# Optimization experiments

Hardware: AMD Instinct MI355X
Metric: run time of the kernel (lower is better)

The kernel has to match this reference:

```python
import jax, jax.numpy as jnp
import numpy as np

B, L, D = 2, 2048, 1024
H = 16
C = 128            # chunk_size
N = L // C         # num chunks
SCALE = float(np.sqrt(D))  # softmax_scale = sqrt(d_model)


def setup_inputs() -> dict:
    key = jax.random.key(0)
    ks = jax.random.split(key, 5)
    return {
        "x": jax.random.normal(ks[0], (B, L, D), dtype=jnp.float32),
        "w_qkv": jax.random.normal(ks[1], (D, 3 * D), dtype=jnp.float32) * (1.0 / np.sqrt(D)),
        "b_qkv": jax.random.normal(ks[2], (3 * D,), dtype=jnp.float32) * 0.02,
        "w_o": jax.random.normal(ks[3], (D, D), dtype=jnp.float32) * (1.0 / np.sqrt(D)),
        "b_o": jax.random.normal(ks[4], (D,), dtype=jnp.float32) * 0.02,
    }


def reference(x, w_qkv, b_qkv, w_o, b_o):
    b, l, d = x.shape
    hd = d // H
    qkv = x @ w_qkv + b_qkv                         # (B,L,3D)
    q, k, v = jnp.split(qkv, 3, axis=-1)
    q = q.reshape(b, l, H, hd)
    k = k.reshape(b, l, H, hd)
    v = v.reshape(b, l, H, hd)

    q_chunks = q.reshape(b, N, C, H, hd)
    k_chunks = k.reshape(b, N, C, H, hd)
    # mean_pool over the chunk dim
    q_pool = q_chunks.mean(axis=2)                  # (B,N,H,hd)
    k_pool = k_chunks.mean(axis=2)

    token2chunk = jnp.einsum('blhd,bnhd->bhln', q, k_pool)          # (B,H,L,N)
    chunk2token = jnp.einsum('bnhd,bnchd->bhnc', q_pool, k_chunks)  # (B,H,N,C)
    # outer product over (n,c) -> full (B,H,L,L) score matrix
    A = token2chunk[..., :, None] * chunk2token[:, :, None, :, :]   # (B,H,L,N,C)
    A = A.reshape(b, H, l, l)

    # direct intra-chunk attention overwrites the diagonal blocks
    direct = jnp.einsum('bnqhd,bnkhd->bhnqk', q_chunks, k_chunks)   # (B,H,N,C,C)
    A6 = A.reshape(b, H, N, C, N, C)
    eye = jnp.eye(N, dtype=bool)[:, None, :, None]                  # (N,1,N,1)
    A6 = jnp.where(eye, direct[:, :, :, :, None, :], A6)
    A = A6.reshape(b, H, l, l)

    # causal mask applied multiplicatively (masked scores become 0, NOT -inf)
    causal = jnp.tril(jnp.ones((l, l), dtype=bool))
    A = jnp.where(causal, A, 0.0) / SCALE
    A = jax.nn.softmax(A, axis=-1)

    out = jnp.einsum('bhqv,bvhd->bhqd', A, v)       # (B,H,L,hd)
    out = out.transpose(0, 2, 1, 3).reshape(b, l, d)
    return out @ w_o + b_o
```

## Files before the change

kernel.cpp:

```cpp
#include <hip/hip_runtime.h>
#include <math.h>

#define B_   2
#define L_   2048
#define D_   1024
#define H_   16
#define HD_  64
#define C_   128
#define N_   16
#define INV_SCALE 0.03125f
#define SCL2 0.0450842200f

typedef _Float16 h8 __attribute__((ext_vector_type(8)));
typedef _Float16 h4 __attribute__((ext_vector_type(4)));
typedef float    f4 __attribute__((ext_vector_type(4)));

#define MFMA16(a, b, c) __builtin_amdgcn_mfma_f32_16x16x32_f16((a), (b), (c), 0, 0, 0)

#if __has_builtin(__builtin_amdgcn_exp2f)
#define EXP2(x) __builtin_amdgcn_exp2f(x)
#else
#define EXP2(x) exp2f(x)
#endif

__device__ __forceinline__ void gl_lds16(const void* g, void* l) {
  __builtin_amdgcn_global_load_lds(
      (const __attribute__((address_space(1))) void*)g,
      (__attribute__((address_space(3))) void*)l, 16, 0, 0);
}

#define SBAR()  do { __builtin_amdgcn_sched_barrier(0); \
                     __builtin_amdgcn_s_barrier();      \
                     __builtin_amdgcn_sched_barrier(0); } while (0)
#define LGKM0() do { asm volatile("s_waitcnt lgkmcnt(0)" ::: "memory"); \
                     __builtin_amdgcn_sched_barrier(0); } while (0)
#define VMW(n)  do { asm volatile("s_waitcnt vmcnt(" #n ")" ::: "memory"); \
                     __builtin_amdgcn_sched_barrier(0); } while (0)

__global__ __launch_bounds__(256) void prep_kernel(
    const float* __restrict__ X, _Float16* __restrict__ Xh,
    const float* __restrict__ Wq, _Float16* __restrict__ WqT,
    const float* __restrict__ Wo, _Float16* __restrict__ WoT)
{
  __shared__ float ts[32][36];
  const int tid = threadIdx.x;
  const int id = blockIdx.x;
  if (id < 4096) {
    int i = id * 1024 + tid * 4;
    float4 v = *(const float4*)(X + i);
    h4 o = { (_Float16)v.x, (_Float16)v.y, (_Float16)v.z, (_Float16)v.w };
    *(h4*)(Xh + i) = o;
    return;
  }
  const float* W; _Float16* WT; int Nc, bx, by;
  if (id < 7168) {
    int idx = id - 4096;
    W = Wq; WT = WqT; Nc = 3072; bx = idx % 96; by = idx / 96;
  } else {
    int idx = id - 7168;
    W = Wo; WT = WoT; Nc = 1024; bx = idx & 31; by = idx >> 5;
  }
  const int n0 = bx * 32, k0 = by * 32;
  {
    int kr = tid >> 3, nc4 = (tid & 7) * 4;
    float4 v = *(const float4*)&W[(size_t)(k0 + kr) * Nc + n0 + nc4];
    ts[kr][nc4+0] = v.x; ts[kr][nc4+1] = v.y; ts[kr][nc4+2] = v.z; ts[kr][nc4+3] = v.w;
  }
  __syncthreads();
  {
    int nr = tid >> 3, kc4 = (tid & 7) * 4;
    h4 o = { (_Float16)ts[kc4+0][nr], (_Float16)ts[kc4+1][nr],
             (_Float16)ts[kc4+2][nr], (_Float16)ts[kc4+3][nr] };
    *(h4*)&WT[(size_t)(n0 + nr) * 1024 + k0 + kc4] = o;
  }
}

__global__ __launch_bounds__(512, 2) void qkv256_kernel(
    const _Float16* __restrict__ A, const _Float16* __restrict__ Bt,
    const float* __restrict__ bias,
    _Float16* __restrict__ Qh, _Float16* __restrict__ Kh, _Float16* __restrict__ VT,
    float* __restrict__ QP, float* __restrict__ KP, float* __restrict__ VCS)
{
  __shared__ __align__(16) _Float16 As[2][16384];
  __shared__ __align__(16) _Float16 Bs[2][12288];

  const int tid = threadIdx.x;
  const int w = tid >> 6, lane = tid & 63;
  const int q = lane >> 4, r = lane & 15, r7 = r & 7;
  const int wm = w >> 2, wn = w & 3;

  const int id = blockIdx.x, xcd = id & 7, slot = id >> 3;
  const int m0 = ((xcd >> 1) * 4 + (slot & 3)) * 256;
  const int n0 = ((xcd & 1) * 8 + (slot >> 2)) * 192;

  const int srow = tid >> 3;
  const int spart = (tid & 7) ^ (srow & 7);
  const _Float16* Asrc = A  + (size_t)(m0 + srow) * 1024 + spart * 8;
  const _Float16* Bsrc = Bt + (size_t)(n0 + srow) * 1024 + spart * 8;
  const int ldst = w * 512;

  const int aoffb = (wm * 128 + r) * 64;
  const int boffb = (wn * 48 + r) * 64;
  const int k0s = (q ^ r7) << 3;
  const int k1s = ((4 + q) ^ r7) << 3;

  auto stA = [&](int cc, int ko, int qq) {
    gl_lds16(Asrc + (size_t)qq * 65536 + ko, &As[cc][qq * 4096 + ldst]);
  };
  auto stB = [&](int cc, int ko, int qq) {
    gl_lds16(Bsrc + (size_t)qq * 65536 + ko, &Bs[cc][qq * 4096 + ldst]);
  };

  f4 acc[8][3];
  #pragma unroll
  for (int m = 0; m < 8; ++m)
    #pragma unroll
    for (int n = 0; n < 3; ++n) acc[m][n] = (f4){0.f, 0.f, 0.f, 0.f};

  stB(0, 0, 0); stB(0, 0, 1); stB(0, 0, 2);
  stA(0, 0, 0); stA(0, 0, 2); stA(0, 0, 1); stA(0, 0, 3);
  VMW(2);
  SBAR();

  for (int t = 0; t < 16; ++t) {
    const int c = t & 1;
    const _Float16* __restrict__ Ab = As[c];
    const _Float16* __restrict__ Bb = Bs[c];
    const int kt = (t + 1) << 6;
    const bool pf = (t < 15);
    h8 af[4], bf[3];

    #pragma unroll
    for (int m = 0; m < 4; ++m) af[m] = *(const h8*)&Ab[aoffb + m * 1024 + k0s];
    #pragma unroll
    for (int n = 0; n < 3; ++n) bf[n] = *(const h8*)&Bb[boffb + n * 1024 + k0s];
    if (pf) { stB(c ^ 1, kt, 0); stB(c ^ 1, kt, 1); }
    SBAR();
    LGKM0();
    __builtin_amdgcn_s_setprio(1);
    #pragma unroll
    for (int m = 0; m < 4; ++m)
      #pragma unroll
      for (int n = 0; n < 3; ++n) acc[m][n] = MFMA16(af[m], bf[n], acc[m][n]);
    __builtin_amdgcn_s_setprio(0);
    __builtin_amdgcn_sched_barrier(0);
    if (pf) { VMW(2); } else { VMW(0); }
    SBAR();

    #pragma unroll
    for (int m = 0; m < 4; ++m) af[m] = *(const h8*)&Ab[aoffb + (4 + m) * 1024 + k0s];
    if (pf) { stB(c ^ 1, kt, 2); stA(c ^ 1, kt, 0); }
    SBAR();
    LGKM0();
    __builtin_amdgcn_s_setprio(1);
    #pragma unroll
    for (int m = 0; m < 4; ++m)
      #pragma unroll
      for (int n = 0; n < 3; ++n) acc[4 + m][n] = MFMA16(af[m], bf[n], acc[4 + m][n]);
    __builtin_amdgcn_s_setprio(0);
    __builtin_amdgcn_sched_barrier(0);
    SBAR();

    #pragma unroll
    for (int m = 0; m < 4; ++m) af[m] = *(const h8*)&Ab[aoffb + m * 1024 + k1s];
    #pragma unroll
    for (int n = 0; n < 3; ++n) bf[n] = *(const h8*)&Bb[boffb + n * 1024 + k1s];
    if (pf) { stA(c ^ 1, kt, 2); stA(c ^ 1, kt, 1); }
    SBAR();
    LGKM0();
    __builtin_amdgcn_s_setprio(1);
    #pragma unroll
    for (int m = 0; m < 4; ++m)
      #pragma unroll
      for (int n = 0; n < 3; ++n) acc[m][n] = MFMA16(af[m], bf[n], acc[m][n]);
    __builtin_amdgcn_s_setprio(0);
    __builtin_amdgcn_sched_barrier(0);
    SBAR();

    #pragma unroll
    for (int m = 0; m < 4; ++m) af[m] = *(const h8*)&Ab[aoffb + (4 + m) * 1024 + k1s];
    if (pf) {
      stA(c ^ 1, kt, 3);
      VMW(2);
    }
    SBAR();
    LGKM0();
    __builtin_amdgcn_s_setprio(1);
    #pragma unroll
    for (int m = 0; m < 4; ++m)
      #pragma unroll
      for (int n = 0; n < 3; ++n) acc[4 + m][n] = MFMA16(af[m], bf[n], acc[4 + m][n]);
    __builtin_amdgcn_s_setprio(0);
    __builtin_amdgcn_sched_barrier(0);
    SBAR();
  }

  const int rb = m0 + wm * 128;
  const int b2 = rb >> 11;
  const int nch = (rb & 2047) >> 7;
  #pragma unroll
  for (int tc = 0; tc < 3; ++tc) {
    const int gn = n0 + wn * 48 + tc * 16 + r;
    const float bj = bias[gn];
    const int which = gn >> 10, rem = gn & 1023;
    const int h2 = rem >> 6, d2 = rem & 63;
    if (which < 2) {
      _Float16* dst = which == 0 ? Qh : Kh;
      #pragma unroll
      for (int m = 0; m < 8; ++m)
        #pragma unroll
        for (int i = 0; i < 4; ++i) {
          const int gm = rb + m * 16 + q * 4 + i;
          const int l2 = gm & 2047;
          dst[(((size_t)(b2 * H_ + h2)) * L_ + l2) * HD_ + d2] =
              (_Float16)(acc[m][tc][i] + bj);
        }
    } else {
      #pragma unroll
      for (int m = 0; m < 8; ++m) {
        const int gm0 = rb + m * 16 + q * 4;
        const int l2 = gm0 & 2047;
        h4 hv = { (_Float16)(acc[m][tc][0] + bj), (_Float16)(acc[m][tc][1] + bj),
                  (_Float16)(acc[m][tc][2] + bj), (_Float16)(acc[m][tc][3] + bj) };
        *(h4*)&VT[((size_t)(b2 * H_ + h2) * HD_ + d2) * L_ + l2] = hv;
      }
    }
    float s2 = 0.f;
    #pragma unroll
    for (int m = 0; m < 8; ++m)
      #pragma unroll
      for (int i = 0; i < 4; ++i) s2 += acc[m][tc][i];
    s2 += __shfl_xor(s2, 16);
    s2 += __shfl_xor(s2, 32);
    if (q == 0) {
      const size_t o = (((size_t)(b2 * H_ + h2)) * N_ + nch) * HD_ + d2;
      if (which == 0)      QP[o] = s2 * (1.f / 128.f) + bj;
      else if (which == 1) KP[o] = s2 * (1.f / 128.f) + bj;
      else                 VCS[o] = s2 + 128.f * bj;
    }
  }
}

template<int MT>
__global__ __launch_bounds__(256, 4) void gemm16_kernel(
    const _Float16* __restrict__ A, const _Float16* __restrict__ Bt,
    const float* __restrict__ bias,
    _Float16* __restrict__ Qh, _Float16* __restrict__ Kh, _Float16* __restrict__ VT,
    float* __restrict__ out,
    float* __restrict__ QP, float* __restrict__ KP, float* __restrict__ VCS,
    int Kd, int mode)
{
  constexpr int SM = MT / 32;
  __shared__ __align__(16) _Float16 As[2][MT * 32];
  __shared__ __align__(16) _Float16 Bs[2][4096];
  __shared__ float cred[2][128];
  const int tid = threadIdx.x;
  const int lane = tid & 63, w = tid >> 6;
  const int q = lane >> 4, r = lane & 15;
  const int mb = (w >> 1) * (MT / 2);
  const int nb = (w & 1) * 64;

  int m0, n0;
  {
    const int id = blockIdx.x;
    const int xcd = id & 7, slot = id >> 3;
    if constexpr (MT == 128) {
      n0 = (xcd * 3 + (slot % 3)) * 128;
      m0 = (slot / 3) * 128;
    } else {
      m0 = (xcd * 8 + (slot >> 3)) * 64;
      n0 = (slot & 7) * 128;
    }
  }

  const int Rr = tid >> 2;
  const int cd = (tid & 3) ^ ((Rr >> 1) & 3);
  const _Float16* Ag = A + (size_t)(m0 + Rr) * Kd + cd * 8;
  const _Float16* Bg = Bt + (size_t)(n0 + Rr) * Kd + cd * 8;
  const size_t rowStep = (size_t)64 * Kd;

  f4 acc[SM][4];
  #pragma unroll
  for (int s = 0; s < SM; ++s)
    #pragma unroll
    for (int t = 0; t < 4; ++t) acc[s][t] = (f4){0.f, 0.f, 0.f, 0.f};

  const int nIter = Kd >> 5;
  const int koff = (q ^ ((r >> 1) & 3)) << 3;

  auto stage = [&](int bf, int kt) {
    _Float16* Asl = &As[bf][w * 512];
    _Float16* Bsl = &Bs[bf][w * 512];
    gl_lds16(Ag + kt, Asl);
    if constexpr (MT == 128) gl_lds16(Ag + kt + rowStep, Asl + 2048);
    gl_lds16(Bg + kt, Bsl);
    gl_lds16(Bg + kt + rowStep, Bsl + 2048);
  };

  stage(0, 0);

  for (int it = 0; it < nIter; ++it) {
    __syncthreads();
    if (it + 1 < nIter) stage((it + 1) & 1, (it + 1) << 5);
    const _Float16* Ab = As[it & 1];
    const _Float16* Bb = Bs[it & 1];
    h8 af[SM], bf4[4];
    #pragma unroll
    for (int s = 0; s < SM; ++s)
      af[s] = *(const h8*)&Ab[(mb + s * 16 + r) * 32 + koff];
    #pragma unroll
    for (int t = 0; t < 4; ++t)
      bf4[t] = *(const h8*)&Bb[(nb + t * 16 + r) * 32 + koff];
    #pragma unroll
    for (int s = 0; s < SM; ++s)
      #pragma unroll
      for (int t = 0; t < 4; ++t)
        acc[s][t] = MFMA16(af[s], bf4[t], acc[s][t]);
  }

  if (mode == 0) {
    #pragma unroll
    for (int t = 0; t < 4; ++t) {
      int gn = n0 + nb + t * 16 + r;
      float bj = bias[gn];
      int which = gn >> 10, rem = gn & 1023;
      int h2 = rem >> 6, d2 = rem & 63;
      if (which < 2) {
        _Float16* dst = which == 0 ? Qh : Kh;
        #pragma unroll
        for (int s = 0; s < SM; ++s)
          #pragma unroll
          for (int i = 0; i < 4; ++i) {
            int gm = m0 + mb + s * 16 + q * 4 + i;
            int b2 = gm >> 11, l2 = gm & 2047;
            dst[(((size_t)(b2 * H_ + h2)) * L_ + l2) * HD_ + d2] =
                (_Float16)(acc[s][t][i] + bj);
          }
      } else {
        #pragma unroll
        for (int s = 0; s < SM; ++s) {
          int gm0 = m0 + mb + s * 16 + q * 4;
          int b2 = gm0 >> 11, l2 = gm0 & 2047;
          h4 hv = { (_Float16)(acc[s][t][0] + bj), (_Float16)(acc[s][t][1] + bj),
                    (_Float16)(acc[s][t][2] + bj), (_Float16)(acc[s][t][3] + bj) };
          *(h4*)&VT[((size_t)(b2 * H_ + h2) * HD_ + d2) * L_ + l2] = hv;
        }
      }
    }
    float colsum[4];
    #pragma unroll
    for (int t = 0; t < 4; ++t) {
      float s2 = 0.f;
      #pragma unroll
      for (int s = 0; s < SM; ++s)
        #pragma unroll
        for (int i = 0; i < 4; ++i) s2 += acc[s][t][i];
      s2 += __shfl_xor(s2, 16);
      s2 += __shfl_xor(s2, 32);
      colsum[t] = s2;
    }
    if (q == 0) {
      #pragma unroll
      for (int t = 0; t < 4; ++t)
        cred[w >> 1][nb + t * 16 + r] = colsum[t];
    }
    __syncthreads();
    if (tid < 128) {
      int jj = tid;
      float ssum = cred[0][jj] + cred[1][jj];
      int gn = n0 + jj;
      float bj = bias[gn];
      int which = gn >> 10, rem = gn & 1023;
      int h2 = rem >> 6, d2 = rem & 63;
      int b2 = m0 >> 11, nch = (m0 & 2047) >> 7;
      size_t o = (((size_t)(b2 * H_ + h2)) * N_ + nch) * HD_ + d2;
      if (which == 0)      QP[o] = ssum * (1.f / 128.f) + bj;
      else if (which == 1) KP[o] = ssum * (1.f / 128.f) + bj;
      else                 VCS[o] = ssum + 128.f * bj;
    }
  } else {
    #pragma unroll
    for (int t = 0; t < 4; ++t) {
      int gn = n0 + nb + t * 16 + r;
      float bj = bias[gn];
      #pragma unroll
      for (int s = 0; s < SM; ++s)
        #pragma unroll
        for (int i = 0; i < 4; ++i) {
          int gm = m0 + mb + s * 16 + q * 4 + i;
          out[(size_t)gm * 1024 + gn] = acc[s][t][i] + bj;
        }
    }
  }
}

__global__ __launch_bounds__(128) void pool2_kernel(
    const float* __restrict__ QP, const _Float16* __restrict__ Kh,
    const float* __restrict__ VCS,
    float* __restrict__ C2T, float* __restrict__ C2TMX, float* __restrict__ C2TMN,
    float* __restrict__ CSUF)
{
  __shared__ float qp_s[64];
  __shared__ float red[4];
  if (blockIdx.x >= 512) {
    int bh = blockIdx.x - 512, d = threadIdx.x;
    if (d < 64) {
      float run = 0.f;
      for (int n = N_ - 1; n >= 0; --n) {
        size_t o = ((size_t)bh * N_ + n) * HD_ + d;
        CSUF[o] = run;
        run += VCS[o];
      }
    }
    return;
  }
  int bh = blockIdx.x >> 4, n = blockIdx.x & 15, tid = threadIdx.x;
  int w = tid >> 6, lane = tid & 63;
  if (tid < 64) qp_s[tid] = QP[((size_t)bh * N_ + n) * HD_ + tid];
  const _Float16* kr = Kh + (((size_t)bh * L_) + n * C_ + tid) * HD_;
  h8 kv[8];
  #pragma unroll
  for (int c8 = 0; c8 < 8; ++c8) kv[c8] = *(const h8*)(kr + c8 * 8);
  __syncthreads();
  float s = 0.f;
  #pragma unroll
  for (int c8 = 0; c8 < 8; ++c8)
    #pragma unroll
    for (int j = 0; j < 8; ++j)
      s = fmaf((float)kv[c8][j], qp_s[c8 * 8 + j], s);
  C2T[((size_t)bh * N_ + n) * C_ + tid] = s;
  float mx = s, mn = s;
  #pragma unroll
  for (int st = 1; st <= 32; st <<= 1) {
    mx = fmaxf(mx, __shfl_xor(mx, st));
    mn = fminf(mn, __shfl_xor(mn, st));
  }
  if (lane == 0) { red[w * 2] = mx; red[w * 2 + 1] = mn; }
  __syncthreads();
  if (tid == 0) {
    C2TMX[bh * N_ + n] = fmaxf(red[0], red[2]);
    C2TMN[bh * N_ + n] = fminf(red[1], red[3]);
  }
}

__global__ __launch_bounds__(512, 4) void attn4_kernel(
    const _Float16* __restrict__ Qh, const _Float16* __restrict__ Kh,
    const _Float16* __restrict__ VT,
    const float* __restrict__ C2T, const float* __restrict__ C2TMX,
    const float* __restrict__ C2TMN, const float* __restrict__ CSUF,
    const float* __restrict__ KP, _Float16* __restrict__ AOh)
{
  __shared__ __align__(16) _Float16 buf0[8192];
  __shared__ __align__(16) _Float16 buf1[8192];
  __shared__ __align__(16) _Float16 buf2[8192];
  __shared__ __align__(16) _Float16 kp_s[1024];
  __shared__ __align__(16) float c2t_s[2][128];

  const int tid = threadIdx.x;
  const int w = tid >> 6, lane = tid & 63;
  const int q = lane >> 4, r = lane & 15;
  const int r7 = r & 7;
  const int id = blockIdx.x;
  const int bh = ((id & 7) << 2) + ((id >> 3) & 3);
  const int nq = 15 - (id >> 5);
  const int l0 = nq * 128;
  const int rowA = l0 + w * 16 + r;
  const int pcw = w * 16 + r;
  const size_t bhL = (size_t)bh * L_;
  const int b2 = bh >> 4, h2 = bh & 15;

  auto stageV = [&](_Float16* buf, int n) {
    #pragma unroll
    for (int j2 = 0; j2 < 2; ++j2) {
      int f = j2 * 512 + tid;
      int d = f >> 4, p = f & 15;
      int c16 = p ^ (d & 7);
      gl_lds16(VT + ((size_t)bh * HD_ + d) * L_ + n * C_ + c16 * 8,
               buf + (size_t)(j2 * 512 + w * 64) * 8);
    }
  };
  auto stageK = [&](_Float16* buf, int n) {
    #pragma unroll
    for (int j2 = 0; j2 < 2; ++j2) {
      int f = j2 * 512 + tid;
      int c = f >> 3, p = f & 7;
      int ck = p ^ (c & 7);
      gl_lds16(Kh + (bhL + n * C_ + c) * HD_ + ck * 8,
               buf + (size_t)(j2 * 512 + w * 64) * 8);
    }
  };
  auto stageC = [&](int bf, int n) {
    if (tid < 32)
      gl_lds16(C2T + ((size_t)bh * N_ + n) * C_ + tid * 4, &c2t_s[bf][0]);
  };

  if (tid < 256) {
    int n4 = tid >> 4, d4 = (tid & 15) * 4;
    float4 kpv = *(const float4*)&KP[((size_t)bh * N_ + n4) * HD_ + d4];
    int sd = ((((d4 >> 3) ^ (n4 & 7)) << 3) | (d4 & 7));
    h4 hv = { (_Float16)kpv.x, (_Float16)kpv.y, (_Float16)kpv.z, (_Float16)kpv.w };
    *(h4*)&kp_s[n4 * 64 + sd] = hv;
  }
  h8 qa0 = *(const h8*)(Qh + (bhL + rowA) * HD_ + q * 8);
  h8 qa1 = *(const h8*)(Qh + (bhL + rowA) * HD_ + 32 + q * 8);
  float mxL = C2TMX[bh * N_ + r];
  float mnL = C2TMN[bh * N_ + r];
  stageK(buf0, nq);
  stageV(buf2, nq);
  if (nq >= 1) stageC(0, nq - 1);
  __syncthreads();

  f4 tvacc = (f4){0.f, 0.f, 0.f, 0.f};
  {
    h8 kpa0 = *(const h8*)&kp_s[r * 64 + ((q ^ r7) << 3)];
    h8 kpa1 = *(const h8*)&kp_s[r * 64 + (((4 + q) ^ r7) << 3)];
    tvacc = MFMA16(kpa0, qa0, tvacc);
    tvacc = MFMA16(kpa1, qa1, tvacc);
  }
  float tvs[4];
  #pragma unroll
  for (int i = 0; i < 4; ++i) tvs[i] = tvacc[i] * SCL2;

  float pm = -1e30f;
  #pragma unroll
  for (int i = 0; i < 4; ++i) {
    int n = q * 4 + i;
    float mx = __shfl(mxL, n);
    float mn = __shfl(mnL, n);
    float cm = fmaxf(tvs[i] * mx, tvs[i] * mn);
    pm = (n < nq) ? fmaxf(pm, cm) : pm;
  }
  pm = fmaxf(pm, __shfl_xor(pm, 16));
  pm = fmaxf(pm, __shfl_xor(pm, 32));

  f4 sc[8];
  #pragma unroll
  for (int u = 0; u < 8; ++u) sc[u] = (f4){0.f, 0.f, 0.f, 0.f};
  {
    h8 kc0 = *(const h8*)&buf0[r * 64 + ((q ^ r7) << 3)];
    h8 kc1 = *(const h8*)&buf0[r * 64 + (((4 + q) ^ r7) << 3)];
    #pragma unroll
    for (int u = 0; u < 8; ++u) {
      h8 kn0, kn1;
      if (u < 7) {
        kn0 = *(const h8*)&buf0[((u + 1) * 16 + r) * 64 + ((q ^ r7) << 3)];
        kn1 = *(const h8*)&buf0[((u + 1) * 16 + r) * 64 + (((4 + q) ^ r7) << 3)];
      }
      sc[u] = MFMA16(kc0, qa0, sc[u]);
      sc[u] = MFMA16(kc1, qa1, sc[u]);
      kc0 = kn0; kc1 = kn1;
    }
  }

  float rm = -1e30f;
  #pragma unroll
  for (int u = 0; u < 8; ++u)
    #pragma unroll
    for (int i = 0; i < 4; ++i) {
      int lcol = u * 16 + q * 4 + i;
      float v = sc[u][i] * SCL2;
      v = (lcol <= pcw) ? v : -1e30f;
      sc[u][i] = v;
      rm = fmaxf(rm, v);
    }
  rm = fmaxf(rm, __shfl_xor(rm, 16));
  rm = fmaxf(rm, __shfl_xor(rm, 32));

  const float M = fmaxf(fmaxf(pm, rm), 0.f);
  const float e0 = EXP2(-M);

  __syncthreads();

  _Float16* pw = (w < 4) ? (buf0 + w * 2048) : (buf1 + (w - 4) * 2048);
  const int pwbase = r * 128 + ((q & 1) << 2);
  float csl = 0.f;
  #pragma unroll
  for (int u = 0; u < 8; ++u) {
    h4 pv4;
    #pragma unroll
    for (int i = 0; i < 4; ++i) {
      float v = sc[u][i];
      float p = (v > -1e29f) ? EXP2(v - M) : 0.f;
      csl += p;
      pv4[i] = (_Float16)p;
    }
    *(h4*)&pw[pwbase + ((((u << 1) | (q >> 1)) ^ r7) << 3)] = pv4;
  }
  csl += __shfl_xor(csl, 16);
  csl += __shfl_xor(csl, 32);
  float den = csl;

  f4 oacc[4], sacc[4];
  #pragma unroll
  for (int t = 0; t < 4; ++t) {
    oacc[t] = (f4){0.f, 0.f, 0.f, 0.f};
    sacc[t] = (f4){0.f, 0.f, 0.f, 0.f};
  }
  {
    h8 pcur = *(const h8*)&pw[r * 128 + ((q ^ r7) << 3)];
    h8 vcur[4];
    #pragma unroll
    for (int t = 0; t < 4; ++t)
      vcur[t] = *(const h8*)&buf2[(t * 16 + r) * 128 + ((q ^ r7) << 3)];
    #pragma unroll
    for (int s = 0; s < 4; ++s) {
      h8 pnxt; h8 vnxt[4];
      if (s < 3) {
        pnxt = *(const h8*)&pw[r * 128 + ((((s + 1) * 4 + q) ^ r7) << 3)];
        #pragma unroll
        for (int t = 0; t < 4; ++t)
          vnxt[t] = *(const h8*)&buf2[(t * 16 + r) * 128 + ((((s + 1) * 4 + q) ^ r7) << 3)];
      }
      h8 mk;
      #pragma unroll
      for (int j2 = 0; j2 < 8; ++j2)
        mk[j2] = (_Float16)((s * 32 + q * 8 + j2 > pcw) ? 1.f : 0.f);
      #pragma unroll
      for (int t = 0; t < 4; ++t) {
        oacc[t] = MFMA16(pcur, vcur[t], oacc[t]);
        sacc[t] = MFMA16(mk, vcur[t], sacc[t]);
      }
      pcur = pnxt;
      #pragma unroll
      for (int t = 0; t < 4; ++t) vcur[t] = vnxt[t];
    }
  }

  __syncthreads();
  if (nq >= 1) stageV(buf1, nq - 1);

  float dsum = 0.f;
  const float negM = -M;
  for (int n = nq - 1; n >= 0; --n) {
    const int k = nq - 1 - n;
    const _Float16* curb = (k & 1) ? buf2 : buf1;
    __syncthreads();
    if (n >= 1) {
      stageV((k & 1) ? buf1 : buf2, n - 1);
      stageC((k + 1) & 1, n - 1);
    }
    int i0 = n & 3;
    float tvx = i0 == 0 ? tvs[0] : i0 == 1 ? tvs[1] : i0 == 2 ? tvs[2] : tvs[3];
    float tvn = __shfl(tvx, ((n >> 2) << 4) + r);
    const float* c2p = c2t_s[k & 1];

    f4 cca = *(const f4*)&c2p[q * 8];
    f4 ccb = *(const f4*)&c2p[q * 8 + 4];
    h8 vcur[4];
    #pragma unroll
    for (int t = 0; t < 4; ++t)
      vcur[t] = *(const h8*)&curb[(t * 16 + r) * 128 + ((q ^ r7) << 3)];

    #pragma unroll
    for (int s = 0; s < 4; ++s) {
      f4 can, cbn; h8 vnxt[4];
      if (s < 3) {
        can = *(const f4*)&c2p[(s + 1) * 32 + q * 8];
        cbn = *(const f4*)&c2p[(s + 1) * 32 + q * 8 + 4];
        #pragma unroll
        for (int t = 0; t < 4; ++t)
          vnxt[t] = *(const h8*)&curb[(t * 16 + r) * 128 + ((((s + 1) * 4 + q) ^ r7) << 3)];
      }
      float p0 = EXP2(fmaf(tvn, cca[0], negM)), p1 = EXP2(fmaf(tvn, cca[1], negM));
      float p2 = EXP2(fmaf(tvn, cca[2], negM)), p3 = EXP2(fmaf(tvn, cca[3], negM));
      float p4 = EXP2(fmaf(tvn, ccb[0], negM)), p5 = EXP2(fmaf(tvn, ccb[1], negM));
      float p6 = EXP2(fmaf(tvn, ccb[2], negM)), p7 = EXP2(fmaf(tvn, ccb[3], negM));
      dsum += p0 + p1 + p2 + p3 + p4 + p5 + p6 + p7;
      h8 pa = { (_Float16)p0, (_Float16)p1, (_Float16)p2, (_Float16)p3,
                (_Float16)p4, (_Float16)p5, (_Float16)p6, (_Float16)p7 };
      #pragma unroll
      for (int t = 0; t < 4; ++t)
        oacc[t] = MFMA16(pa, vcur[t], oacc[t]);
      cca = can; ccb = cbn;
      #pragma unroll
      for (int t = 0; t < 4; ++t) vcur[t] = vnxt[t];
    }
  }
  dsum += __shfl_xor(dsum, 16);
  dsum += __shfl_xor(dsum, 32);
  den += dsum;

  int cnt = (L_ - 1) - rowA;
  den += e0 * (float)cnt;
  float e0r[4], dnr[4];
  #pragma unroll
  for (int i = 0; i < 4; ++i) {
    e0r[i] = __shfl(e0,  (q << 2) + i);
    dnr[i] = __shfl(den, (q << 2) + i);
  }
  #pragma unroll
  for (int t = 0; t < 4; ++t) {
    int d = t * 16 + r;
    float csf = CSUF[((size_t)bh * N_ + nq) * HD_ + d];
    #pragma unroll
    for (int i = 0; i < 4; ++i) {
      int row = l0 + w * 16 + q * 4 + i;
      float suffix = sacc[t][i] + csf;
      float o = (oacc[t][i] + e0r[i] * suffix) / dnr[i];
      AOh[((size_t)b2 * L_ + row) * D_ + h2 * HD_ + d] = (_Float16)o;
    }
  }
}

extern "C" void kernel_launch(void* const* d_in, const int* in_sizes, int n_in,
                              void* d_out, int out_size, void* d_ws, size_t ws_size,
                              hipStream_t stream)
{
  (void)in_sizes; (void)n_in; (void)out_size; (void)ws_size;
  const float* x     = (const float*)d_in[0];
  const float* w_qkv = (const float*)d_in[1];
  const float* b_qkv = (const float*)d_in[2];
  const float* w_o   = (const float*)d_in[3];
  const float* b_o   = (const float*)d_in[4];
  float* out = (float*)d_out;

  char* p = (char*)d_ws;
  _Float16* xh   = (_Float16*)p; p += (size_t)4194304 * 2;
  _Float16* wqT  = (_Float16*)p; p += (size_t)3145728 * 2;
  _Float16* woT  = (_Float16*)p; p += (size_t)1048576 * 2;
  _Float16* Qh   = (_Float16*)p; p += (size_t)4194304 * 2;
  _Float16* Kh   = (_Float16*)p; p += (size_t)4194304 * 2;
  _Float16* VT   = (_Float16*)p; p += (size_t)4194304 * 2;
  _Float16* AOh  = (_Float16*)p; p += (size_t)4194304 * 2;
  float*    C2T  = (float*)p;    p += (size_t)65536 * 4;
  float*    QP   = (float*)p;    p += (size_t)32768 * 4;
  float*    KP   = (float*)p;    p += (size_t)32768 * 4;
  float*    VCS  = (float*)p;    p += (size_t)32768 * 4;
  float*    CSUF = (float*)p;    p += (size_t)32768 * 4;
  float*    MXa  = (float*)p;    p += (size_t)512 * 4;
  float*    MNa  = (float*)p;    p += (size_t)512 * 4;

  prep_kernel<<<8192, 256, 0, stream>>>(x, xh, w_qkv, wqT, w_o, woT);
  qkv256_kernel<<<256, 512, 0, stream>>>(
      xh, wqT, b_qkv, Qh, Kh, VT, QP, KP, VCS);
  pool2_kernel<<<544, 128, 0, stream>>>(QP, Kh, VCS, C2T, MXa, MNa, CSUF);
  attn4_kernel<<<512, 512, 0, stream>>>(
      Qh, Kh, VT, C2T, MXa, MNa, CSUF, KP, AOh);
  gemm16_kernel<64><<<512, 256, 0, stream>>>(
      AOh, woT, b_o, nullptr, nullptr, nullptr, out, nullptr, nullptr, nullptr, D_, 1);
}
```

Baseline: 171.4 us.

## Rebalance QKV prefetch schedule, trim gemm epilogue, reorder attention block order

The QKV GEMM loop now issues its next-tile global-to-LDS stage loads earlier: all three B stages go out in the first phase and the A stages are pulled forward. The wait count is adjusted to match. The gemm16 kernel drops its unused mode-0 epilogue and extra parameters, which may cut register and LDS use. The attention kernel's chunk order changes from strictly heaviest-first to heavy-then-light. That changes how causal work is spread across dispatch waves and may hurt tail balance.

```diff
diff --git a/kernel.cpp b/kernel.cpp
--- a/kernel.cpp
+++ b/kernel.cpp
@@ -134,7 +134,7 @@
     for (int m = 0; m < 4; ++m) af[m] = *(const h8*)&Ab[aoffb + m * 1024 + k0s];
     #pragma unroll
     for (int n = 0; n < 3; ++n) bf[n] = *(const h8*)&Bb[boffb + n * 1024 + k0s];
-    if (pf) { stB(c ^ 1, kt, 0); stB(c ^ 1, kt, 1); }
+    if (pf) { stB(c ^ 1, kt, 0); stB(c ^ 1, kt, 1); stB(c ^ 1, kt, 2); }
     SBAR();
     LGKM0();
     __builtin_amdgcn_s_setprio(1);
@@ -144,12 +144,12 @@
       for (int n = 0; n < 3; ++n) acc[m][n] = MFMA16(af[m], bf[n], acc[m][n]);
     __builtin_amdgcn_s_setprio(0);
     __builtin_amdgcn_sched_barrier(0);
-    if (pf) { VMW(2); } else { VMW(0); }
+    if (pf) { VMW(3); } else { VMW(0); }
     SBAR();
 
     #pragma unroll
     for (int m = 0; m < 4; ++m) af[m] = *(const h8*)&Ab[aoffb + (4 + m) * 1024 + k0s];
-    if (pf) { stB(c ^ 1, kt, 2); stA(c ^ 1, kt, 0); }
+    if (pf) { stA(c ^ 1, kt, 0); stA(c ^ 1, kt, 2); stA(c ^ 1, kt, 1); }
     SBAR();
     LGKM0();
     __builtin_amdgcn_s_setprio(1);
@@ -165,7 +165,7 @@
     for (int m = 0; m < 4; ++m) af[m] = *(const h8*)&Ab[aoffb + m * 1024 + k1s];
     #pragma unroll
     for (int n = 0; n < 3; ++n) bf[n] = *(const h8*)&Bb[boffb + n * 1024 + k1s];
-    if (pf) { stA(c ^ 1, kt, 2); stA(c ^ 1, kt, 1); }
+    if (pf) { stA(c ^ 1, kt, 3); }
     SBAR();
     LGKM0();
     __builtin_amdgcn_s_setprio(1);
@@ -180,7 +180,6 @@
     #pragma unroll
     for (int m = 0; m < 4; ++m) af[m] = *(const h8*)&Ab[aoffb + (4 + m) * 1024 + k1s];
     if (pf) {
-      stA(c ^ 1, kt, 3);
       VMW(2);
     }
     SBAR();
@@ -244,16 +243,11 @@
 template<int MT>
 __global__ __launch_bounds__(256, 4) void gemm16_kernel(
     const _Float16* __restrict__ A, const _Float16* __restrict__ Bt,
-    const float* __restrict__ bias,
-    _Float16* __restrict__ Qh, _Float16* __restrict__ Kh, _Float16* __restrict__ VT,
-    float* __restrict__ out,
-    float* __restrict__ QP, float* __restrict__ KP, float* __restrict__ VCS,
-    int Kd, int mode)
+    const float* __restrict__ bias, float* __restrict__ out, int Kd)
 {
   constexpr int SM = MT / 32;
   __shared__ __align__(16) _Float16 As[2][MT * 32];
   __shared__ __align__(16) _Float16 Bs[2][4096];
-  __shared__ float cred[2][128];
   const int tid = threadIdx.x;
   const int lane = tid & 63, w = tid >> 6;
   const int q = lane >> 4, r = lane & 15;
@@ -264,13 +258,8 @@
   {
     const int id = blockIdx.x;
     const int xcd = id & 7, slot = id >> 3;
-    if constexpr (MT == 128) {
-      n0 = (xcd * 3 + (slot % 3)) * 128;
-      m0 = (slot / 3) * 128;
-    } else {
-      m0 = (xcd * 8 + (slot >> 3)) * 64;
-      n0 = (slot & 7) * 128;
-    }
+    m0 = (xcd * 8 + (slot >> 3)) * 64;
+    n0 = (slot & 7) * 128;
   }
 
   const int Rr = tid >> 2;
@@ -318,79 +307,17 @@
         acc[s][t] = MFMA16(af[s], bf4[t], acc[s][t]);
   }
 
-  if (mode == 0) {
-    #pragma unroll
-    for (int t = 0; t < 4; ++t) {
-      int gn = n0 + nb + t * 16 + r;
-      float bj = bias[gn];
-      int which = gn >> 10, rem = gn & 1023;
-      int h2 = rem >> 6, d2 = rem & 63;
-      if (which < 2) {
-        _Float16* dst = which == 0 ? Qh : Kh;
-        #pragma unroll
-        for (int s = 0; s < SM; ++s)
-          #pragma unroll
-          for (int i = 0; i < 4; ++i) {
-            int gm = m0 + mb + s * 16 + q * 4 + i;
-            int b2 = gm >> 11, l2 = gm & 2047;
-            dst[(((size_t)(b2 * H_ + h2)) * L_ + l2) * HD_ + d2] =
-                (_Float16)(acc[s][t][i] + bj);
-          }
-      } else {
-        #pragma unroll
-        for (int s = 0; s < SM; ++s) {
-          int gm0 = m0 + mb + s * 16 + q * 4;
-          int b2 = gm0 >> 11, l2 = gm0 & 2047;
-          h4 hv = { (_Float16)(acc[s][t][0] + bj), (_Float16)(acc[s][t][1] + bj),
-                    (_Float16)(acc[s][t][2] + bj), (_Float16)(acc[s][t][3] + bj) };
-          *(h4*)&VT[((size_t)(b2 * H_ + h2) * HD_ + d2) * L_ + l2] = hv;
-        }
+  #pragma unroll
+  for (int t = 0; t < 4; ++t) {
+    int gn = n0 + nb + t * 16 + r;
+    float bj = bias[gn];
+    #pragma unroll
+    for (int s = 0; s < SM; ++s)
+      #pragma unroll
+      for (int i = 0; i < 4; ++i) {
+        int gm = m0 + mb + s * 16 + q * 4 + i;
+        out[(size_t)gm * 1024 + gn] = acc[s][t][i] + bj;
       }
-    }
-    float colsum[4];
-    #pragma unroll
-    for (int t = 0; t < 4; ++t) {
-      float s2 = 0.f;
-      #pragma unroll
-      for (int s = 0; s < SM; ++s)
-        #pragma unroll
-        for (int i = 0; i < 4; ++i) s2 += acc[s][t][i];
-      s2 += __shfl_xor(s2, 16);
-      s2 += __shfl_xor(s2, 32);
-      colsum[t] = s2;
-    }
-    if (q == 0) {
-      #pragma unroll
-      for (int t = 0; t < 4; ++t)
-        cred[w >> 1][nb + t * 16 + r] = colsum[t];
-    }
-    __syncthreads();
-    if (tid < 128) {
-      int jj = tid;
-      float ssum = cred[0][jj] + cred[1][jj];
-      int gn = n0 + jj;
-      float bj = bias[gn];
-      int which = gn >> 10, rem = gn & 1023;
-      int h2 = rem >> 6, d2 = rem & 63;
-      int b2 = m0 >> 11, nch = (m0 & 2047) >> 7;
-      size_t o = (((size_t)(b2 * H_ + h2)) * N_ + nch) * HD_ + d2;
-      if (which == 0)      QP[o] = ssum * (1.f / 128.f) + bj;
-      else if (which == 1) KP[o] = ssum * (1.f / 128.f) + bj;
-      else                 VCS[o] = ssum + 128.f * bj;
-    }
-  } else {
-    #pragma unroll
-    for (int t = 0; t < 4; ++t) {
-      int gn = n0 + nb + t * 16 + r;
-      float bj = bias[gn];
-      #pragma unroll
-      for (int s = 0; s < SM; ++s)
-        #pragma unroll
-        for (int i = 0; i < 4; ++i) {
-          int gm = m0 + mb + s * 16 + q * 4 + i;
-          out[(size_t)gm * 1024 + gn] = acc[s][t][i] + bj;
-        }
-    }
   }
 }
 
@@ -462,7 +389,8 @@
   const int r7 = r & 7;
   const int id = blockIdx.x;
   const int bh = ((id & 7) << 2) + ((id >> 3) & 3);
-  const int nq = 15 - (id >> 5);
+  const int s5 = id >> 5;
+  const int nq = (s5 < 8) ? (15 - s5) : (s5 - 8);
   const int l0 = nq * 128;
   const int rowA = l0 + w * 16 + r;
   const int pcw = w * 16 + r;
@@ -737,5 +665,5 @@
   attn4_kernel<<<512, 512, 0, stream>>>(
       Qh, Kh, VT, C2T, MXa, MNa, CSUF, KP, AOh);
   gemm16_kernel<64><<<512, 256, 0, stream>>>(
-      AOh, woT, b_o, nullptr, nullptr, nullptr, out, nullptr, nullptr, nullptr, D_, 1);
+      AOh, woT, b_o, out, D_);
 }
```

After: 168.7 us. About the same (-1.6%).
